# Optimization experiments

Hardware: AMD Instinct MI355X
Metric: run time of the kernel (lower is better)

Reference implementation:

```python
import jax, jax.numpy as jnp
import numpy as np

# Regularized layout for the per-batch masked attention:
#   batch_size B=8, each batch has NF=2048 'fill' points followed by NK=4096 'keep' points.
B, NF, NK = 8, 2048, 4096
C_IN, C_KQ, C_OUT = 256, 64, 256


def setup_inputs() -> dict:
    key = jax.random.key(0)
    ks = jax.random.split(key, 7)
    N = B * (NF + NK)
    features = jax.random.normal(ks[0], (N, C_IN), dtype=jnp.float32)
    # keep flag: 0 for fill points, 1 for keep points, per batch (fill-first layout)
    flag = jnp.tile(jnp.concatenate([jnp.zeros(NF, jnp.int32), jnp.ones(NK, jnp.int32)]), B)
    s = 1.0 / np.sqrt(C_IN)
    Wq = jax.random.normal(ks[1], (C_KQ, C_IN), jnp.float32) * s
    bq = jnp.zeros((C_KQ,), jnp.float32)
    Wk = jax.random.normal(ks[2], (C_KQ, C_IN), jnp.float32) * s
    bk = jnp.zeros((C_KQ,), jnp.float32)
    Wv = jax.random.normal(ks[3], (C_OUT, C_IN), jnp.float32) * s
    bv = jnp.zeros((C_OUT,), jnp.float32)
    return {"features": features, "keep_flag": flag,
            "Wq": Wq, "bq": bq, "Wk": Wk, "bk": bk, "Wv": Wv, "bv": bv}


def reference(features, keep_flag, Wq, bq, Wk, bk, Wv, bv):
    # features: [N, C_IN]; keep_flag encodes the fill/keep split, which in this
    # regular layout is: first NF rows of each batch are fill, remaining NK are keep.
    del keep_flag  # structure is encoded in the layout (fill-first per batch)
    f = features.reshape(B, NF + NK, C_IN)
    fill = f[:, :NF]             # [B, NF, C_IN]
    keep = f[:, NF:]             # [B, NK, C_IN]
    q = fill @ Wq.T + bq         # [B, NF, C_KQ]
    k = keep @ Wk.T + bk         # [B, NK, C_KQ]
    v = keep @ Wv.T + bv         # [B, NK, C_OUT]
    ratio = np.sqrt(C_KQ).astype(np.float32)
    scores = jnp.einsum('bfd,bkd->bfk', q, k) / ratio   # [B, NF, NK]
    attn = jax.nn.softmax(scores, axis=-1)
    out_fill = jnp.einsum('bfk,bkc->bfc', attn, v)      # [B, NF, C_OUT]
    # keep rows pass through unchanged (only fill rows are overwritten)
    out = jnp.concatenate([out_fill, keep], axis=1)
    return out.reshape(B * (NF + NK), C_OUT)
```

## Files before the change

### kernel.cpp

```cpp
#include <hip/hip_runtime.h>
#include <hip/hip_bf16.h>

#define BATCHES 8
#define NFILL 2048
#define NKEEP 4096
#define SEQLEN 6144
#define CIN 256
#define CKQ 64
#define COUT 256

#define KSC 0.18033688011112042f
#define KOFF -11.541560327111707f

typedef __bf16 bf16_t;
typedef float f32x4 __attribute__((ext_vector_type(4)));
typedef bf16_t bf16x8 __attribute__((ext_vector_type(8)));

__device__ inline void cvt8_store(bf16_t* dst, float4 a, float4 b) {
  bf16x8 v;
  v[0] = (bf16_t)a.x; v[1] = (bf16_t)a.y; v[2] = (bf16_t)a.z; v[3] = (bf16_t)a.w;
  v[4] = (bf16_t)b.x; v[5] = (bf16_t)b.y; v[6] = (bf16_t)b.z; v[7] = (bf16_t)b.w;
  *(bf16x8*)dst = v;
}

__global__ __launch_bounds__(256) void gemm_qk(
    const float* __restrict__ feat, const float* __restrict__ Wq,
    const float* __restrict__ bq, const float* __restrict__ Wk,
    const float* __restrict__ bk, bf16_t* __restrict__ Qw,
    bf16_t* __restrict__ Kw) {
  __shared__ bf16_t Xs[64][72];
  __shared__ bf16_t Ws[64][72];

  const int QBLOCKS = BATCHES * NFILL / 64;
  const bool isK = blockIdx.x >= QBLOCKS;
  const int mb = isK ? blockIdx.x - QBLOCKS : blockIdx.x;
  const float* W = isK ? Wk : Wq;
  const float* bias = isK ? bk : bq;
  bf16_t* outp = isK ? Kw : Qw;
  const int rpb_shift = isK ? 12 : 11;
  const int row_off = isK ? NFILL : 0;

  const int t = threadIdx.x;
  const int lane = t & 63;
  const int wv = t >> 6;
  const int l16 = lane & 15;
  const int quad = lane >> 4;

  const int lr = t >> 2;
  const int koff = (t & 3) << 4;
  const int mrow = mb * 64 + lr;
  const int batch = mrow >> rpb_shift;
  const int ridx = mrow & ((1 << rpb_shift) - 1);
  const float* xptr = feat + ((long)(batch * SEQLEN + row_off + ridx)) * CIN + koff;
  const float* wptr = W + ((long)lr) * CIN + koff;

  f32x4 acc[4];
#pragma unroll
  for (int nb = 0; nb < 4; nb++) acc[nb] = f32x4{0.f, 0.f, 0.f, 0.f};

  for (int k0 = 0; k0 < CIN; k0 += 64) {
    float4 x0 = *(const float4*)(xptr + k0);
    float4 x1 = *(const float4*)(xptr + k0 + 4);
    float4 x2 = *(const float4*)(xptr + k0 + 8);
    float4 x3 = *(const float4*)(xptr + k0 + 12);
    float4 w0 = *(const float4*)(wptr + k0);
    float4 w1 = *(const float4*)(wptr + k0 + 4);
    float4 w2 = *(const float4*)(wptr + k0 + 8);
    float4 w3 = *(const float4*)(wptr + k0 + 12);
    __syncthreads();
    cvt8_store(&Xs[lr][koff], x0, x1);
    cvt8_store(&Xs[lr][koff + 8], x2, x3);
    cvt8_store(&Ws[lr][koff], w0, w1);
    cvt8_store(&Ws[lr][koff + 8], w2, w3);
    __syncthreads();
#pragma unroll
    for (int ks = 0; ks < 2; ks++) {
      bf16x8 afrag = *(const bf16x8*)&Xs[wv * 16 + l16][ks * 32 + quad * 8];
#pragma unroll
      for (int nb = 0; nb < 4; nb++) {
        bf16x8 bfrag = *(const bf16x8*)&Ws[nb * 16 + l16][ks * 32 + quad * 8];
        acc[nb] = __builtin_amdgcn_mfma_f32_16x16x32_bf16(afrag, bfrag, acc[nb], 0, 0, 0);
      }
    }
  }

#pragma unroll
  for (int nb = 0; nb < 4; nb++) {
    const int n = nb * 16 + l16;
    const float bb = bias[n];
#pragma unroll
    for (int r = 0; r < 4; r++) {
      const int m = mb * 64 + wv * 16 + quad * 4 + r;
      outp[(long)m * CKQ + n] = (bf16_t)(acc[nb][r] + bb);
    }
  }
}

__global__ __launch_bounds__(256) void gemm_v(
    const float* __restrict__ feat, const float* __restrict__ Wv,
    const float* __restrict__ bv, bf16_t* __restrict__ Vw,
    float* __restrict__ outp) {
  __shared__ bf16_t Xs[64][264];
  __shared__ bf16_t Ws[64][72];
  __shared__ float Cs[64][68];

  const int mb = blockIdx.x;
  const int t = threadIdx.x;
  const int lane = t & 63;
  const int wv = t >> 6;
  const int l16 = lane & 15;
  const int quad = lane >> 4;

  const int lr = t >> 2;
  const int koff = (t & 3) << 4;

  const int grow = mb * 64 + lr;
  const int batch = grow >> 12;
  const int ridx = grow & 4095;
  const float* xptr = feat + ((long)(batch * SEQLEN + NFILL + ridx)) * CIN;
  float4* orow = (float4*)(outp + ((long)(batch * SEQLEN + NFILL + ridx)) * COUT);

#pragma unroll
  for (int j = 0; j < 4; j++) {
    const int c = koff + j * 64;
    float4 x0 = *(const float4*)(xptr + c);
    float4 x1 = *(const float4*)(xptr + c + 4);
    float4 x2 = *(const float4*)(xptr + c + 8);
    float4 x3 = *(const float4*)(xptr + c + 12);
    cvt8_store(&Xs[lr][c], x0, x1);
    cvt8_store(&Xs[lr][c + 8], x2, x3);
    orow[(c >> 2) + 0] = x0;
    orow[(c >> 2) + 1] = x1;
    orow[(c >> 2) + 2] = x2;
    orow[(c >> 2) + 3] = x3;
  }
  __syncthreads();

  const int vb = (mb * 64) >> 12;
  const int key0base = (mb * 64) & 4095;

  for (int nt = 0; nt < 4; nt++) {
    const int n0 = nt * 64;
    f32x4 acc[4];
#pragma unroll
    for (int nb = 0; nb < 4; nb++) acc[nb] = f32x4{0.f, 0.f, 0.f, 0.f};

    for (int k0 = 0; k0 < CIN; k0 += 64) {
      const float* wptr = Wv + ((long)(n0 + lr)) * CIN + k0 + koff;
      float4 w0 = *(const float4*)(wptr);
      float4 w1 = *(const float4*)(wptr + 4);
      float4 w2 = *(const float4*)(wptr + 8);
      float4 w3 = *(const float4*)(wptr + 12);
      __syncthreads();
      cvt8_store(&Ws[lr][koff], w0, w1);
      cvt8_store(&Ws[lr][koff + 8], w2, w3);
      __syncthreads();
#pragma unroll
      for (int ks = 0; ks < 2; ks++) {
        bf16x8 afrag = *(const bf16x8*)&Xs[wv * 16 + l16][k0 + ks * 32 + quad * 8];
#pragma unroll
        for (int nb = 0; nb < 4; nb++) {
          bf16x8 bfrag = *(const bf16x8*)&Ws[nb * 16 + l16][ks * 32 + quad * 8];
          acc[nb] = __builtin_amdgcn_mfma_f32_16x16x32_bf16(afrag, bfrag, acc[nb], 0, 0, 0);
        }
      }
    }

    __syncthreads();
#pragma unroll
    for (int nb = 0; nb < 4; nb++) {
      const float bb = bv[n0 + nb * 16 + l16];
#pragma unroll
      for (int r = 0; r < 4; r++)
        Cs[wv * 16 + quad * 4 + r][nb * 16 + l16] = acc[nb][r] + bb;
    }
    __syncthreads();
    const int c = t >> 2;
    const int seg = t & 3;
    bf16_t tmp[16];
#pragma unroll
    for (int i = 0; i < 16; i++) tmp[i] = (bf16_t)Cs[seg * 16 + i][c];
    bf16_t* dst = Vw + ((long)(vb * COUT + n0 + c)) * NKEEP + key0base + seg * 16;
    *(uint4*)dst = *(uint4*)tmp;
    *(uint4*)(dst + 8) = *(uint4*)(tmp + 8);
  }
}

__global__ __launch_bounds__(256) void attn_kernel(
    const bf16_t* __restrict__ Q, const bf16_t* __restrict__ K,
    const bf16_t* __restrict__ Vt, float* __restrict__ outp) {
  __shared__ bf16_t Ks[2][64][72];
  __shared__ bf16_t Ps[64][72];
  __shared__ float Lsh[64];

  const int qt = blockIdx.x;
  const int b = blockIdx.y;
  const int t = threadIdx.x;
  const int lane = t & 63;
  const int wv = t >> 6;
  const int l16 = lane & 15;
  const int quad = lane >> 4;

  const int krow = t >> 2;
  const int kcol = (t & 3) << 4;

  const bf16_t* kbase = K + (long)b * NKEEP * CKQ;
  const int c0 = wv * 64;
  const bf16_t* vlane =
      Vt + ((long)(b * COUT + c0 + l16)) * NKEEP + quad * 8;

  bf16x8 qfrag[2];
  {
    const bf16_t* qrow = Q + ((long)(b * NFILL + qt * 64 + wv * 16 + l16)) * CKQ;
#pragma unroll
    for (int ks = 0; ks < 2; ks++)
      qfrag[ks] = *(const bf16x8*)(qrow + ks * 32 + quad * 8);
  }

  f32x4 oacc[4][4];
#pragma unroll
  for (int m = 0; m < 4; m++)
#pragma unroll
    for (int ct = 0; ct < 4; ct++) oacc[m][ct] = f32x4{0.f, 0.f, 0.f, 0.f};
  float rsum[4] = {0.f, 0.f, 0.f, 0.f};

  uint4 kreg0, kreg1;
  bf16x8 vA[8], vB[8];

  {
    const bf16_t* ksrc = kbase + (long)krow * CKQ + kcol;
    uint4 k0 = *(const uint4*)ksrc;
    uint4 k1 = *(const uint4*)(ksrc + 8);
#pragma unroll
    for (int ct = 0; ct < 4; ct++)
#pragma unroll
      for (int ks = 0; ks < 2; ks++)
        vA[ct * 2 + ks] = *(const bf16x8*)(vlane + (long)ct * 16 * NKEEP + ks * 32);
    *(uint4*)&Ks[0][krow][kcol] = k0;
    *(uint4*)&Ks[0][krow][kcol + 8] = k1;
  }

#define ATTN_TILE(BUF, VCUR, VNEXT, TV)                                         \
  {                                                                             \
    __syncthreads(); \
    const int tn = ((TV) + 1 < 64) ? (TV) + 1 : 63;                             \
    {                                                                           \
      const bf16_t* ksrc = kbase + ((long)(tn * 64 + krow)) * CKQ + kcol;       \
      kreg0 = *(const uint4*)ksrc;                                              \
      kreg1 = *(const uint4*)(ksrc + 8);                                        \
      const bf16_t* vsrc = vlane + (long)tn * 64;                               \
      _Pragma("unroll") for (int ct = 0; ct < 4; ct++)                          \
          _Pragma("unroll") for (int ks = 0; ks < 2; ks++)                      \
              VNEXT[ct * 2 + ks] =                                              \
          *(const bf16x8*)(vsrc + (long)ct * 16 * NKEEP + ks * 32);             \
    }                                                                           \
    f32x4 sacc[4];                                                              \
    _Pragma("unroll") for (int nb = 0; nb < 4; nb++)                            \
        sacc[nb] = f32x4{0.f, 0.f, 0.f, 0.f};                                   \
    _Pragma("unroll") for (int ks = 0; ks < 2; ks++) {                          \
      _Pragma("unroll") for (int nb = 0; nb < 4; nb++) {                        \
        bf16x8 kfrag = *(const bf16x8*)&Ks[BUF][nb * 16 + l16][ks * 32 + quad * 8]; \
        sacc[nb] = __builtin_amdgcn_mfma_f32_16x16x32_bf16(qfrag[ks], kfrag,    \
                                                           sacc[nb], 0, 0, 0); \
      }                                                                         \
    }                                                                           \
    _Pragma("unroll") for (int nb = 0; nb < 4; nb++) {                          \
      _Pragma("unroll") for (int r = 0; r < 4; r++) {                           \
        const float p = __builtin_exp2f(fmaf(sacc[nb][r], KSC, KOFF));          \
        rsum[r] += p;                                                           \
        Ps[wv * 16 + quad * 4 + r][nb * 16 + l16] = (bf16_t)p;                  \
      }                                                                         \
    }                                                                           \
    asm volatile("s_waitcnt lgkmcnt(0)\n\ts_barrier" ::: "memory");      \
    _Pragma("unroll") for (int ks = 0; ks < 2; ks++) {                          \
      _Pragma("unroll") for (int m = 0; m < 4; m++) {                           \
        bf16x8 pfrag = *(const bf16x8*)&Ps[m * 16 + l16][ks * 32 + quad * 8];   \
        _Pragma("unroll") for (int ct = 0; ct < 4; ct++)                        \
            oacc[m][ct] = __builtin_amdgcn_mfma_f32_16x16x32_bf16(              \
                pfrag, VCUR[ct * 2 + ks], oacc[m][ct], 0, 0, 0);                \
      }                                                                         \
    }                                                                           \
    *(uint4*)&Ks[BUF ^ 1][krow][kcol] = kreg0;                                  \
    *(uint4*)&Ks[BUF ^ 1][krow][kcol + 8] = kreg1;                              \
  }

#pragma unroll 1
  for (int tv = 0; tv < 64; tv += 2) {
    ATTN_TILE(0, vA, vB, tv)
    ATTN_TILE(1, vB, vA, tv + 1)
  }
#undef ATTN_TILE

#pragma unroll
  for (int off = 1; off < 16; off <<= 1)
#pragma unroll
    for (int r = 0; r < 4; r++) rsum[r] += __shfl_xor(rsum[r], off, 64);
  if (l16 == 0) {
#pragma unroll
    for (int r = 0; r < 4; r++) Lsh[wv * 16 + quad * 4 + r] = rsum[r];
  }
  __syncthreads();

  float rl[4][4];
#pragma unroll
  for (int m = 0; m < 4; m++)
#pragma unroll
    for (int r = 0; r < 4; r++) rl[m][r] = 1.0f / Lsh[m * 16 + quad * 4 + r];

  const long obase = ((long)(b * SEQLEN + qt * 64)) * COUT + c0;
#pragma unroll
  for (int m = 0; m < 4; m++)
#pragma unroll
    for (int ct = 0; ct < 4; ct++)
#pragma unroll
      for (int r = 0; r < 4; r++)
        outp[obase + (long)(m * 16 + quad * 4 + r) * COUT + ct * 16 + l16] =
            oacc[m][ct][r] * rl[m][r];
}

extern "C" void kernel_launch(void* const* d_in, const int* in_sizes, int n_in,
                              void* d_out, int out_size, void* d_ws, size_t ws_size,
                              hipStream_t stream) {
  const float* feat = (const float*)d_in[0];
  const float* Wq = (const float*)d_in[2];
  const float* bq = (const float*)d_in[3];
  const float* Wk = (const float*)d_in[4];
  const float* bk = (const float*)d_in[5];
  const float* Wv = (const float*)d_in[6];
  const float* bv = (const float*)d_in[7];
  float* outp = (float*)d_out;

  bf16_t* Qw = (bf16_t*)d_ws;
  bf16_t* Kw = Qw + (size_t)BATCHES * NFILL * CKQ;
  bf16_t* Vw = Kw + (size_t)BATCHES * NKEEP * CKQ;

  gemm_qk<<<dim3(768), 256, 0, stream>>>(feat, Wq, bq, Wk, bk, Qw, Kw);
  gemm_v<<<dim3(512), 256, 0, stream>>>(feat, Wv, bv, Vw, outp);
  attn_kernel<<<dim3(NFILL / 64, BATCHES), 256, 0, stream>>>(Qw, Kw, Vw, outp);
}
```

Baseline: 215.6 us.

## Fuse Q/K/V projections into one kernel and halve attention query tile

Merges the Q/K and V projection kernels into a single launch in which keep-row blocks compute K and then V from one swizzled shared-memory copy of the input rows, so the keep features are read once instead of twice. The shared tiles use an XOR swizzle to avoid LDS bank conflicts and hold the full 256-wide K dimension. The attention kernel now takes 32 query rows per block instead of 64. Each wave computes scores for its own 16-key slice, and row sums are reduced across waves through shared memory. This doubles the attention grid for better CU occupancy, but each block's K/V tile loads now serve half as many queries.

```diff
diff --git a/kernel.cpp b/kernel.cpp
--- a/kernel.cpp
+++ b/kernel.cpp
@@ -23,163 +23,144 @@
   *(bf16x8*)dst = v;
 }
 
-__global__ __launch_bounds__(256) void gemm_qk(
+__device__ inline int sw(int row, int chunk) {
+  return row * 256 + ((chunk ^ (row & 7)) << 3);
+}
+
+__global__ __launch_bounds__(256) void proj_kernel(
     const float* __restrict__ feat, const float* __restrict__ Wq,
     const float* __restrict__ bq, const float* __restrict__ Wk,
-    const float* __restrict__ bk, bf16_t* __restrict__ Qw,
-    bf16_t* __restrict__ Kw) {
-  __shared__ bf16_t Xs[64][72];
-  __shared__ bf16_t Ws[64][72];
-
-  const int QBLOCKS = BATCHES * NFILL / 64;
-  const bool isK = blockIdx.x >= QBLOCKS;
-  const int mb = isK ? blockIdx.x - QBLOCKS : blockIdx.x;
-  const float* W = isK ? Wk : Wq;
-  const float* bias = isK ? bk : bq;
-  bf16_t* outp = isK ? Kw : Qw;
-  const int rpb_shift = isK ? 12 : 11;
-  const int row_off = isK ? NFILL : 0;
+    const float* __restrict__ bk, const float* __restrict__ Wv,
+    const float* __restrict__ bv, bf16_t* __restrict__ Qw,
+    bf16_t* __restrict__ Kw, bf16_t* __restrict__ Vw,
+    float* __restrict__ outp) {
+  __shared__ __align__(16) unsigned char smem[65536];
+  bf16_t* Xs = (bf16_t*)smem;
+  bf16_t* Ws = (bf16_t*)(smem + 32768);
+  float* Cs = (float*)(smem + 32768);
 
   const int t = threadIdx.x;
   const int lane = t & 63;
   const int wv = t >> 6;
   const int l16 = lane & 15;
   const int quad = lane >> 4;
-
   const int lr = t >> 2;
-  const int koff = (t & 3) << 4;
-  const int mrow = mb * 64 + lr;
-  const int batch = mrow >> rpb_shift;
-  const int ridx = mrow & ((1 << rpb_shift) - 1);
-  const float* xptr = feat + ((long)(batch * SEQLEN + row_off + ridx)) * CIN + koff;
-  const float* wptr = W + ((long)lr) * CIN + koff;
-
-  f32x4 acc[4];
-#pragma unroll
-  for (int nb = 0; nb < 4; nb++) acc[nb] = f32x4{0.f, 0.f, 0.f, 0.f};
-
-  for (int k0 = 0; k0 < CIN; k0 += 64) {
-    float4 x0 = *(const float4*)(xptr + k0);
-    float4 x1 = *(const float4*)(xptr + k0 + 4);
-    float4 x2 = *(const float4*)(xptr + k0 + 8);
-    float4 x3 = *(const float4*)(xptr + k0 + 12);
-    float4 w0 = *(const float4*)(wptr + k0);
-    float4 w1 = *(const float4*)(wptr + k0 + 4);
-    float4 w2 = *(const float4*)(wptr + k0 + 8);
-    float4 w3 = *(const float4*)(wptr + k0 + 12);
-    __syncthreads();
-    cvt8_store(&Xs[lr][koff], x0, x1);
-    cvt8_store(&Xs[lr][koff + 8], x2, x3);
-    cvt8_store(&Ws[lr][koff], w0, w1);
-    cvt8_store(&Ws[lr][koff + 8], w2, w3);
-    __syncthreads();
-#pragma unroll
-    for (int ks = 0; ks < 2; ks++) {
-      bf16x8 afrag = *(const bf16x8*)&Xs[wv * 16 + l16][ks * 32 + quad * 8];
-#pragma unroll
-      for (int nb = 0; nb < 4; nb++) {
-        bf16x8 bfrag = *(const bf16x8*)&Ws[nb * 16 + l16][ks * 32 + quad * 8];
-        acc[nb] = __builtin_amdgcn_mfma_f32_16x16x32_bf16(afrag, bfrag, acc[nb], 0, 0, 0);
-      }
-    }
-  }
-
-#pragma unroll
-  for (int nb = 0; nb < 4; nb++) {
-    const int n = nb * 16 + l16;
-    const float bb = bias[n];
-#pragma unroll
-    for (int r = 0; r < 4; r++) {
-      const int m = mb * 64 + wv * 16 + quad * 4 + r;
-      outp[(long)m * CKQ + n] = (bf16_t)(acc[nb][r] + bb);
-    }
-  }
-}
-
-__global__ __launch_bounds__(256) void gemm_v(
-    const float* __restrict__ feat, const float* __restrict__ Wv,
-    const float* __restrict__ bv, bf16_t* __restrict__ Vw,
-    float* __restrict__ outp) {
-  __shared__ bf16_t Xs[64][264];
-  __shared__ bf16_t Ws[64][72];
-  __shared__ float Cs[64][68];
-
-  const int mb = blockIdx.x;
-  const int t = threadIdx.x;
-  const int lane = t & 63;
-  const int wv = t >> 6;
-  const int l16 = lane & 15;
-  const int quad = lane >> 4;
-
-  const int lr = t >> 2;
-  const int koff = (t & 3) << 4;
-
-  const int grow = mb * 64 + lr;
-  const int batch = grow >> 12;
-  const int ridx = grow & 4095;
-  const float* xptr = feat + ((long)(batch * SEQLEN + NFILL + ridx)) * CIN;
-  float4* orow = (float4*)(outp + ((long)(batch * SEQLEN + NFILL + ridx)) * COUT);
+  const int jc = t & 3;
+
+  const bool isFill = blockIdx.x < 256;
+  int batch, ridx;
+  if (isFill) {
+    const int g = blockIdx.x * 64 + lr;
+    batch = g >> 11; ridx = g & 2047;
+  } else {
+    const int g = (blockIdx.x - 256) * 64 + lr;
+    batch = g >> 12; ridx = (g & 4095) + NFILL;
+  }
+  const float* xptr = feat + ((long)(batch * SEQLEN + ridx)) * CIN;
+  const float* W0 = isFill ? Wq : Wk;
+  const float* w0ptr = W0 + (long)lr * CIN;
 
 #pragma unroll
   for (int j = 0; j < 4; j++) {
-    const int c = koff + j * 64;
+    const int c = jc * 16 + j * 64;
+    const int cc = jc * 2 + j * 8;
     float4 x0 = *(const float4*)(xptr + c);
     float4 x1 = *(const float4*)(xptr + c + 4);
     float4 x2 = *(const float4*)(xptr + c + 8);
     float4 x3 = *(const float4*)(xptr + c + 12);
-    cvt8_store(&Xs[lr][c], x0, x1);
-    cvt8_store(&Xs[lr][c + 8], x2, x3);
-    orow[(c >> 2) + 0] = x0;
-    orow[(c >> 2) + 1] = x1;
-    orow[(c >> 2) + 2] = x2;
-    orow[(c >> 2) + 3] = x3;
+    cvt8_store(&Xs[sw(lr, cc)], x0, x1);
+    cvt8_store(&Xs[sw(lr, cc + 1)], x2, x3);
+    float4 w0 = *(const float4*)(w0ptr + c);
+    float4 w1 = *(const float4*)(w0ptr + c + 4);
+    float4 w2 = *(const float4*)(w0ptr + c + 8);
+    float4 w3 = *(const float4*)(w0ptr + c + 12);
+    cvt8_store(&Ws[sw(lr, cc)], w0, w1);
+    cvt8_store(&Ws[sw(lr, cc + 1)], w2, w3);
+    if (!isFill) {
+      float4* orow = (float4*)(outp + ((long)(batch * SEQLEN + ridx)) * COUT);
+      orow[(c >> 2) + 0] = x0;
+      orow[(c >> 2) + 1] = x1;
+      orow[(c >> 2) + 2] = x2;
+      orow[(c >> 2) + 3] = x3;
+    }
   }
   __syncthreads();
 
-  const int vb = (mb * 64) >> 12;
-  const int key0base = (mb * 64) & 4095;
+  {
+    f32x4 acc[4];
+#pragma unroll
+    for (int nb = 0; nb < 4; nb++) acc[nb] = f32x4{0.f, 0.f, 0.f, 0.f};
+#pragma unroll
+    for (int kb = 0; kb < 8; kb++) {
+      bf16x8 af = *(const bf16x8*)&Xs[sw(wv * 16 + l16, kb * 4 + quad)];
+#pragma unroll
+      for (int nb = 0; nb < 4; nb++) {
+        bf16x8 bf = *(const bf16x8*)&Ws[sw(nb * 16 + l16, kb * 4 + quad)];
+        acc[nb] = __builtin_amdgcn_mfma_f32_16x16x32_bf16(af, bf, acc[nb], 0, 0, 0);
+      }
+    }
+    const float* bias = isFill ? bq : bk;
+    bf16_t* dst = isFill ? Qw : Kw;
+    const int mbase =
+        (isFill ? blockIdx.x : (blockIdx.x - 256)) * 64 + wv * 16 + quad * 4;
+#pragma unroll
+    for (int nb = 0; nb < 4; nb++) {
+      const float bb = bias[nb * 16 + l16];
+#pragma unroll
+      for (int r = 0; r < 4; r++)
+        dst[(long)(mbase + r) * CKQ + nb * 16 + l16] = (bf16_t)(acc[nb][r] + bb);
+    }
+  }
+  if (isFill) return;
+
+  const int kb64 = blockIdx.x - 256;
+  const int vb = (kb64 * 64) >> 12;
+  const int key0base = (kb64 * 64) & 4095;
 
   for (int nt = 0; nt < 4; nt++) {
     const int n0 = nt * 64;
+    __syncthreads();
+    {
+      const float* wptr = Wv + ((long)(n0 + lr)) * CIN;
+#pragma unroll
+      for (int j = 0; j < 4; j++) {
+        const int c = jc * 16 + j * 64;
+        const int cc = jc * 2 + j * 8;
+        float4 w0 = *(const float4*)(wptr + c);
+        float4 w1 = *(const float4*)(wptr + c + 4);
+        float4 w2 = *(const float4*)(wptr + c + 8);
+        float4 w3 = *(const float4*)(wptr + c + 12);
+        cvt8_store(&Ws[sw(lr, cc)], w0, w1);
+        cvt8_store(&Ws[sw(lr, cc + 1)], w2, w3);
+      }
+    }
+    __syncthreads();
     f32x4 acc[4];
 #pragma unroll
     for (int nb = 0; nb < 4; nb++) acc[nb] = f32x4{0.f, 0.f, 0.f, 0.f};
-
-    for (int k0 = 0; k0 < CIN; k0 += 64) {
-      const float* wptr = Wv + ((long)(n0 + lr)) * CIN + k0 + koff;
-      float4 w0 = *(const float4*)(wptr);
-      float4 w1 = *(const float4*)(wptr + 4);
-      float4 w2 = *(const float4*)(wptr + 8);
-      float4 w3 = *(const float4*)(wptr + 12);
-      __syncthreads();
-      cvt8_store(&Ws[lr][koff], w0, w1);
-      cvt8_store(&Ws[lr][koff + 8], w2, w3);
-      __syncthreads();
-#pragma unroll
-      for (int ks = 0; ks < 2; ks++) {
-        bf16x8 afrag = *(const bf16x8*)&Xs[wv * 16 + l16][k0 + ks * 32 + quad * 8];
-#pragma unroll
-        for (int nb = 0; nb < 4; nb++) {
-          bf16x8 bfrag = *(const bf16x8*)&Ws[nb * 16 + l16][ks * 32 + quad * 8];
-          acc[nb] = __builtin_amdgcn_mfma_f32_16x16x32_bf16(afrag, bfrag, acc[nb], 0, 0, 0);
-        }
+#pragma unroll
+    for (int kb = 0; kb < 8; kb++) {
+      bf16x8 af = *(const bf16x8*)&Xs[sw(wv * 16 + l16, kb * 4 + quad)];
+#pragma unroll
+      for (int nb = 0; nb < 4; nb++) {
+        bf16x8 bf = *(const bf16x8*)&Ws[sw(nb * 16 + l16, kb * 4 + quad)];
+        acc[nb] = __builtin_amdgcn_mfma_f32_16x16x32_bf16(af, bf, acc[nb], 0, 0, 0);
       }
     }
-
     __syncthreads();
 #pragma unroll
     for (int nb = 0; nb < 4; nb++) {
       const float bb = bv[n0 + nb * 16 + l16];
 #pragma unroll
       for (int r = 0; r < 4; r++)
-        Cs[wv * 16 + quad * 4 + r][nb * 16 + l16] = acc[nb][r] + bb;
+        Cs[(wv * 16 + quad * 4 + r) * 68 + nb * 16 + l16] = acc[nb][r] + bb;
     }
     __syncthreads();
     const int c = t >> 2;
     const int seg = t & 3;
     bf16_t tmp[16];
 #pragma unroll
-    for (int i = 0; i < 16; i++) tmp[i] = (bf16_t)Cs[seg * 16 + i][c];
+    for (int i = 0; i < 16; i++) tmp[i] = (bf16_t)Cs[(seg * 16 + i) * 68 + c];
     bf16_t* dst = Vw + ((long)(vb * COUT + n0 + c)) * NKEEP + key0base + seg * 16;
     *(uint4*)dst = *(uint4*)tmp;
     *(uint4*)(dst + 8) = *(uint4*)(tmp + 8);
@@ -190,8 +171,8 @@
     const bf16_t* __restrict__ Q, const bf16_t* __restrict__ K,
     const bf16_t* __restrict__ Vt, float* __restrict__ outp) {
   __shared__ bf16_t Ks[2][64][72];
-  __shared__ bf16_t Ps[64][72];
-  __shared__ float Lsh[64];
+  __shared__ bf16_t Ps[32][72];
+  __shared__ float Lsh[4][32];
 
   const int qt = blockIdx.x;
   const int b = blockIdx.y;
@@ -206,23 +187,24 @@
 
   const bf16_t* kbase = K + (long)b * NKEEP * CKQ;
   const int c0 = wv * 64;
-  const bf16_t* vlane =
-      Vt + ((long)(b * COUT + c0 + l16)) * NKEEP + quad * 8;
-
-  bf16x8 qfrag[2];
-  {
-    const bf16_t* qrow = Q + ((long)(b * NFILL + qt * 64 + wv * 16 + l16)) * CKQ;
+  const bf16_t* vlane = Vt + ((long)(b * COUT + c0 + l16)) * NKEEP + quad * 8;
+
+  bf16x8 qfrag[2][2];
+#pragma unroll
+  for (int m = 0; m < 2; m++) {
+    const bf16_t* qrow =
+        Q + ((long)(b * NFILL + qt * 32 + m * 16 + l16)) * CKQ;
 #pragma unroll
     for (int ks = 0; ks < 2; ks++)
-      qfrag[ks] = *(const bf16x8*)(qrow + ks * 32 + quad * 8);
-  }
-
-  f32x4 oacc[4][4];
-#pragma unroll
-  for (int m = 0; m < 4; m++)
+      qfrag[m][ks] = *(const bf16x8*)(qrow + ks * 32 + quad * 8);
+  }
+
+  f32x4 oacc[2][4];
+#pragma unroll
+  for (int m = 0; m < 2; m++)
 #pragma unroll
     for (int ct = 0; ct < 4; ct++) oacc[m][ct] = f32x4{0.f, 0.f, 0.f, 0.f};
-  float rsum[4] = {0.f, 0.f, 0.f, 0.f};
+  float rsum[2][4] = {{0.f, 0.f, 0.f, 0.f}, {0.f, 0.f, 0.f, 0.f}};
 
   uint4 kreg0, kreg1;
   bf16x8 vA[8], vB[8];
@@ -240,48 +222,47 @@
     *(uint4*)&Ks[0][krow][kcol + 8] = k1;
   }
 
-#define ATTN_TILE(BUF, VCUR, VNEXT, TV)                                         \
-  {                                                                             \
-    __syncthreads(); \
-    const int tn = ((TV) + 1 < 64) ? (TV) + 1 : 63;                             \
-    {                                                                           \
-      const bf16_t* ksrc = kbase + ((long)(tn * 64 + krow)) * CKQ + kcol;       \
-      kreg0 = *(const uint4*)ksrc;                                              \
-      kreg1 = *(const uint4*)(ksrc + 8);                                        \
-      const bf16_t* vsrc = vlane + (long)tn * 64;                               \
-      _Pragma("unroll") for (int ct = 0; ct < 4; ct++)                          \
-          _Pragma("unroll") for (int ks = 0; ks < 2; ks++)                      \
-              VNEXT[ct * 2 + ks] =                                              \
-          *(const bf16x8*)(vsrc + (long)ct * 16 * NKEEP + ks * 32);             \
-    }                                                                           \
-    f32x4 sacc[4];                                                              \
-    _Pragma("unroll") for (int nb = 0; nb < 4; nb++)                            \
-        sacc[nb] = f32x4{0.f, 0.f, 0.f, 0.f};                                   \
-    _Pragma("unroll") for (int ks = 0; ks < 2; ks++) {                          \
-      _Pragma("unroll") for (int nb = 0; nb < 4; nb++) {                        \
-        bf16x8 kfrag = *(const bf16x8*)&Ks[BUF][nb * 16 + l16][ks * 32 + quad * 8]; \
-        sacc[nb] = __builtin_amdgcn_mfma_f32_16x16x32_bf16(qfrag[ks], kfrag,    \
-                                                           sacc[nb], 0, 0, 0); \
-      }                                                                         \
-    }                                                                           \
-    _Pragma("unroll") for (int nb = 0; nb < 4; nb++) {                          \
-      _Pragma("unroll") for (int r = 0; r < 4; r++) {                           \
-        const float p = __builtin_exp2f(fmaf(sacc[nb][r], KSC, KOFF));          \
-        rsum[r] += p;                                                           \
-        Ps[wv * 16 + quad * 4 + r][nb * 16 + l16] = (bf16_t)p;                  \
-      }                                                                         \
-    }                                                                           \
-    asm volatile("s_waitcnt lgkmcnt(0)\n\ts_barrier" ::: "memory");      \
-    _Pragma("unroll") for (int ks = 0; ks < 2; ks++) {                          \
-      _Pragma("unroll") for (int m = 0; m < 4; m++) {                           \
-        bf16x8 pfrag = *(const bf16x8*)&Ps[m * 16 + l16][ks * 32 + quad * 8];   \
-        _Pragma("unroll") for (int ct = 0; ct < 4; ct++)                        \
-            oacc[m][ct] = __builtin_amdgcn_mfma_f32_16x16x32_bf16(              \
-                pfrag, VCUR[ct * 2 + ks], oacc[m][ct], 0, 0, 0);                \
-      }                                                                         \
-    }                                                                           \
-    *(uint4*)&Ks[BUF ^ 1][krow][kcol] = kreg0;                                  \
-    *(uint4*)&Ks[BUF ^ 1][krow][kcol + 8] = kreg1;                              \
+#define ATTN_TILE(BUF, VCUR, VNEXT, TV)                                          \
+  {                                                                              \
+    asm volatile("s_waitcnt lgkmcnt(0)\n\ts_barrier" ::: "memory");       \
+    const int tn = ((TV) + 1 < 64) ? (TV) + 1 : 63;                              \
+    {                                                                            \
+      const bf16_t* ksrc = kbase + ((long)(tn * 64 + krow)) * CKQ + kcol;        \
+      kreg0 = *(const uint4*)ksrc;                                               \
+      kreg1 = *(const uint4*)(ksrc + 8);                                         \
+      const bf16_t* vsrc = vlane + (long)tn * 64;                                \
+      _Pragma("unroll") for (int ct = 0; ct < 4; ct++)                           \
+          _Pragma("unroll") for (int ks = 0; ks < 2; ks++)                       \
+              VNEXT[ct * 2 + ks] =                                               \
+          *(const bf16x8*)(vsrc + (long)ct * 16 * NKEEP + ks * 32);              \
+    }                                                                            \
+    f32x4 sacc[2];                                                               \
+    sacc[0] = f32x4{0.f, 0.f, 0.f, 0.f};                                         \
+    sacc[1] = f32x4{0.f, 0.f, 0.f, 0.f};                                         \
+    _Pragma("unroll") for (int ks = 0; ks < 2; ks++) {                           \
+      bf16x8 kfrag = *(const bf16x8*)&Ks[BUF][wv * 16 + l16][ks * 32 + quad * 8];\
+      _Pragma("unroll") for (int m = 0; m < 2; m++)                              \
+          sacc[m] = __builtin_amdgcn_mfma_f32_16x16x32_bf16(qfrag[m][ks], kfrag, \
+                                                            sacc[m], 0, 0, 0);  \
+    }                                                                            \
+    _Pragma("unroll") for (int m = 0; m < 2; m++) {                              \
+      _Pragma("unroll") for (int r = 0; r < 4; r++) {                            \
+        const float p = __builtin_exp2f(fmaf(sacc[m][r], KSC, KOFF));            \
+        rsum[m][r] += p;                                                         \
+        Ps[m * 16 + quad * 4 + r][wv * 16 + l16] = (bf16_t)p;                    \
+      }                                                                          \
+    }                                                                            \
+    asm volatile("s_waitcnt lgkmcnt(0)\n\ts_barrier" ::: "memory");       \
+    _Pragma("unroll") for (int ks = 0; ks < 2; ks++) {                           \
+      _Pragma("unroll") for (int m = 0; m < 2; m++) {                            \
+        bf16x8 pfrag = *(const bf16x8*)&Ps[m * 16 + l16][ks * 32 + quad * 8];    \
+        _Pragma("unroll") for (int ct = 0; ct < 4; ct++)                         \
+            oacc[m][ct] = __builtin_amdgcn_mfma_f32_16x16x32_bf16(               \
+                pfrag, VCUR[ct * 2 + ks], oacc[m][ct], 0, 0, 0);                 \
+      }                                                                          \
+    }                                                                            \
+    *(uint4*)&Ks[BUF ^ 1][krow][kcol] = kreg0;                                   \
+    *(uint4*)&Ks[BUF ^ 1][krow][kcol + 8] = kreg1;                               \
   }
 
 #pragma unroll 1
@@ -294,22 +275,30 @@
 #pragma unroll
   for (int off = 1; off < 16; off <<= 1)
 #pragma unroll
-    for (int r = 0; r < 4; r++) rsum[r] += __shfl_xor(rsum[r], off, 64);
+    for (int m = 0; m < 2; m++)
+#pragma unroll
+      for (int r = 0; r < 4; r++) rsum[m][r] += __shfl_xor(rsum[m][r], off, 64);
   if (l16 == 0) {
 #pragma unroll
-    for (int r = 0; r < 4; r++) Lsh[wv * 16 + quad * 4 + r] = rsum[r];
+    for (int m = 0; m < 2; m++)
+#pragma unroll
+      for (int r = 0; r < 4; r++)
+        Lsh[wv][m * 16 + quad * 4 + r] = rsum[m][r];
   }
   __syncthreads();
 
-  float rl[4][4];
-#pragma unroll
-  for (int m = 0; m < 4; m++)
-#pragma unroll
-    for (int r = 0; r < 4; r++) rl[m][r] = 1.0f / Lsh[m * 16 + quad * 4 + r];
-
-  const long obase = ((long)(b * SEQLEN + qt * 64)) * COUT + c0;
-#pragma unroll
-  for (int m = 0; m < 4; m++)
+  float rl[2][4];
+#pragma unroll
+  for (int m = 0; m < 2; m++)
+#pragma unroll
+    for (int r = 0; r < 4; r++) {
+      const int row = m * 16 + quad * 4 + r;
+      rl[m][r] = 1.0f / (Lsh[0][row] + Lsh[1][row] + Lsh[2][row] + Lsh[3][row]);
+    }
+
+  const long obase = ((long)(b * SEQLEN + qt * 32)) * COUT + c0;
+#pragma unroll
+  for (int m = 0; m < 2; m++)
 #pragma unroll
     for (int ct = 0; ct < 4; ct++)
 #pragma unroll
@@ -334,7 +323,7 @@
   bf16_t* Kw = Qw + (size_t)BATCHES * NFILL * CKQ;
   bf16_t* Vw = Kw + (size_t)BATCHES * NKEEP * CKQ;
 
-  gemm_qk<<<dim3(768), 256, 0, stream>>>(feat, Wq, bq, Wk, bk, Qw, Kw);
-  gemm_v<<<dim3(512), 256, 0, stream>>>(feat, Wv, bv, Vw, outp);
-  attn_kernel<<<dim3(NFILL / 64, BATCHES), 256, 0, stream>>>(Qw, Kw, Vw, outp);
-}
+  proj_kernel<<<dim3(768), 256, 0, stream>>>(feat, Wq, bq, Wk, bk, Wv, bv,
+                                             Qw, Kw, Vw, outp);
+  attn_kernel<<<dim3(NFILL / 32, BATCHES), 256, 0, stream>>>(Qw, Kw, Vw, outp);
+}
```

Measured after the change: 259.9 us. +20.5%, slower.
